# Optimization experiments

Hardware: AMD Instinct MI355X
Metric: run time of the kernel (lower is better)

The kernel has to match this reference:

```python
import jax, jax.numpy as jnp
import numpy as np

B, S, D, H = 4, 1024, 1024, 16
DH = D // H  # head dim = 64
NEG = 1e9  # keras Softmax masking constant for fp32


def setup_inputs() -> dict:
    key = jax.random.key(0)
    ks = jax.random.split(key, 7)
    return {
        "inputs": jax.random.normal(ks[0], (B, S, D), jnp.float32),
        "mask": jax.random.randint(ks[1], (B, 1, 1, S), 0, 2) > 0,
        "interaction": jax.random.normal(ks[2], (B, S, S, H), jnp.float32) * 0.1,
        "W_Q": jax.random.normal(ks[3], (D, D), jnp.float32) * 0.02,
        "W_K": jax.random.normal(ks[4], (D, D), jnp.float32) * 0.02,
        "W_V": jax.random.normal(ks[5], (D, D), jnp.float32) * 0.02,
        "W_O": jax.random.normal(ks[6], (D, D), jnp.float32) * 0.02,
    }


def reference(inputs, mask, interaction, W_Q, W_K, W_V, W_O):
    b, s, d = inputs.shape
    def proj(W):
        # [B,S,D] @ [D,D] -> [B,S,H,DH] -> [B,H,S,DH]
        return (inputs @ W).reshape(b, s, H, DH).transpose(0, 2, 1, 3)
    Q, K, V = proj(W_Q), proj(W_K), proj(W_V)
    scores = jnp.einsum("bhqd,bhkd->bhqk", Q, K) / (DH ** 0.5)
    # interaction [B,S,S,H] -> [B,H,S,S], additive bias before softmax
    scores = scores + interaction.transpose(0, 3, 1, 2)
    # keras Softmax(mask=...): add -1e9 where mask is False, softmax over last axis
    scores = jnp.where(mask, scores, scores - NEG)
    attn = jax.nn.softmax(scores, axis=-1)
    hidden = jnp.einsum("bhqk,bhkd->bhqd", attn, V)
    hidden = hidden.transpose(0, 2, 1, 3).reshape(b, s, d)
    return hidden @ W_O
```

## Files before the change

kernel.cpp:

```cpp
#include <hip/hip_runtime.h>
#include <hip/hip_bf16.h>
#include <stdint.h>

#define BDIM 4
#define SDIM 1024
#define DDIM 1024
#define HDIM 16
#define DHDIM 64

typedef __bf16 bf16_t;
typedef __bf16 bf16x8 __attribute__((ext_vector_type(8)));
typedef __bf16 bf16x4 __attribute__((ext_vector_type(4)));
typedef float f32x4 __attribute__((ext_vector_type(4)));

typedef __attribute__((address_space(3))) uint32_t lds_u32;
typedef const __attribute__((address_space(1))) uint32_t glb_u32;

__device__ __forceinline__ void glds16(const void* g, void* l) {
    __builtin_amdgcn_global_load_lds((glb_u32*)g, (lds_u32*)l, 16, 0, 0);
}


__global__ __launch_bounds__(256) void convert_x_kernel(const float* __restrict__ X,
                                                        bf16_t* __restrict__ Xb, int n) {
    int i = (blockIdx.x * 256 + threadIdx.x) * 4;
    if (i >= n) return;
    float4 v = *(const float4*)(X + i);
    bf16x4 o;
    o[0] = (bf16_t)v.x; o[1] = (bf16_t)v.y; o[2] = (bf16_t)v.z; o[3] = (bf16_t)v.w;
    *(bf16x4*)(Xb + i) = o;
}

__global__ __launch_bounds__(256) void transpose_w_kernel(const float* __restrict__ W0,
                                                          const float* __restrict__ W1,
                                                          const float* __restrict__ W2,
                                                          const float* __restrict__ W3,
                                                          bf16_t* __restrict__ Wt) {
    __shared__ float tile[32][33];
    int z = blockIdx.z;
    const float* W = (z == 0) ? W0 : (z == 1) ? W1 : (z == 2) ? W2 : W3;
    bf16_t* dst = Wt + (size_t)z * DDIM * DDIM;
    int bx = blockIdx.x * 32;
    int by = blockIdx.y * 32;
    int x = threadIdx.x & 31, y0 = threadIdx.x >> 5;
#pragma unroll
    for (int i = 0; i < 4; i++) {
        int y = y0 + i * 8;
        tile[y][x] = W[(size_t)(by + y) * DDIM + bx + x];
    }
    __syncthreads();
#pragma unroll
    for (int i = 0; i < 4; i++) {
        int y = y0 + i * 8;
        dst[(size_t)(bx + y) * DDIM + by + x] = (bf16_t)tile[x][y];
    }
}

__global__ __launch_bounds__(1024) void mask_flag_kernel(const unsigned char* __restrict__ mb,
                                                         int* __restrict__ flag) {
    __shared__ int any;
    if (threadIdx.x == 0) any = 0;
    __syncthreads();
    int loc = 0;
    for (int i = threadIdx.x; i < BDIM * SDIM; i += 1024)
        if ((i & 3) && mb[i]) loc = 1;
    if (loc) any = 1;
    __syncthreads();
    if (threadIdx.x == 0) *flag = any ? 1 : 0;
}

template <int MODE>
__global__ __launch_bounds__(256) void gemm_bt_kernel(const bf16_t* __restrict__ A,
                                                      const bf16_t* __restrict__ Bt,
                                                      bf16_t* __restrict__ Qo, bf16_t* __restrict__ Ko,
                                                      bf16_t* __restrict__ Vto, float* __restrict__ Co) {
    __shared__ bf16_t As[128 * 32];
    __shared__ bf16_t Bs[128 * 32];
    const int m0 = blockIdx.x * 128;
    const int n0 = blockIdx.y * 128;
    const int t = threadIdx.x;
    const int lane = t & 63, w = t >> 6;
    const int wm = w & 1, wn = w >> 1;
    const int low = lane & 15, quad = lane >> 4;
    f32x4 acc[4][4] = {};

    const int srow = w * 16 + (lane >> 2);
    const int koff = (lane & 3) * 8;
    const bf16_t* Ag = A + (size_t)(m0 + srow) * DDIM + koff;
    const bf16_t* Bg = Bt + (size_t)(n0 + srow) * DDIM + koff;
    bf16_t* AsW = As + w * 512;
    bf16_t* BsW = Bs + w * 512;

    for (int k0 = 0; k0 < DDIM; k0 += 32) {
        __syncthreads();
        glds16(Ag + k0, AsW);
        glds16(Ag + (size_t)64 * DDIM + k0, AsW + 64 * 32);
        glds16(Bg + k0, BsW);
        glds16(Bg + (size_t)64 * DDIM + k0, BsW + 64 * 32);
        __syncthreads();
        bf16x8 af[4], bv[4];
#pragma unroll
        for (int mt = 0; mt < 4; mt++)
            af[mt] = *(const bf16x8*)(As + (wm * 64 + mt * 16 + low) * 32 + quad * 8);
#pragma unroll
        for (int nt = 0; nt < 4; nt++)
            bv[nt] = *(const bf16x8*)(Bs + (wn * 64 + nt * 16 + low) * 32 + quad * 8);
#pragma unroll
        for (int mt = 0; mt < 4; mt++)
#pragma unroll
            for (int nt = 0; nt < 4; nt++)
                acc[mt][nt] = __builtin_amdgcn_mfma_f32_16x16x32_bf16(af[mt], bv[nt], acc[mt][nt], 0, 0, 0);
    }

#pragma unroll
    for (int mt = 0; mt < 4; mt++) {
#pragma unroll
        for (int nt = 0; nt < 4; nt++) {
#pragma unroll
            for (int r = 0; r < 4; r++) {
                int mrow = m0 + wm * 64 + mt * 16 + quad * 4 + r;
                int ncol = n0 + wn * 64 + nt * 16 + low;
                float vv = acc[mt][nt][r];
                if (MODE == 0) {
                    int which = ncol >> 10, nl = ncol & 1023;
                    int h = nl >> 6, dh = nl & 63;
                    int b = mrow >> 10, s = mrow & 1023;
                    if (which == 0)
                        Qo[((size_t)(b * HDIM + h) * SDIM + s) * DHDIM + dh] = (bf16_t)(vv * 0.125f);
                    else if (which == 1)
                        Ko[((size_t)(b * HDIM + h) * SDIM + s) * DHDIM + dh] = (bf16_t)vv;
                    else
                        Vto[((size_t)(b * HDIM + h) * DHDIM + dh) * SDIM + s] = (bf16_t)vv;
                } else {
                    Co[(size_t)mrow * DDIM + ncol] = vv;
                }
            }
        }
    }
}

__global__ __launch_bounds__(1024, 4) void attn_kernel(const bf16_t* __restrict__ Q,
                                                       const bf16_t* __restrict__ K,
                                                       const bf16_t* __restrict__ Vt,
                                                       const float* __restrict__ inter,
                                                       const unsigned char* __restrict__ maskb,
                                                       const int* __restrict__ flagp,
                                                       bf16_t* __restrict__ hid) {
    constexpr int KS = 20;
    constexpr int HS = 32 * KS + 4;
    __shared__ bf16_t bias_l[2][16 * HS];
    __shared__ bf16_t P[16][16 * 40];
    const int b = blockIdx.y;
    const int q0 = blockIdx.x * 16;
    const int t = threadIdx.x;
    const int w = t >> 6, lane = t & 63;
    const int low = lane & 15, quad = lane >> 4;
    const int h = w;
    const int mstride = (*flagp) ? 1 : 4;

    const int kl = lane >> 1;
    const int hb = (lane & 1) * 8;
    const float* srcQ = inter + ((size_t)(b * SDIM + q0 + w) * SDIM) * HDIM + lane * 8;
    const unsigned char* mb = maskb + (size_t)b * SDIM * mstride;

    const bf16_t* Qb = Q + ((size_t)(b * HDIM + h) * SDIM + q0) * DHDIM;
    bf16x8 qf0 = *(const bf16x8*)(Qb + low * DHDIM + quad * 8);
    bf16x8 qf1 = *(const bf16x8*)(Qb + low * DHDIM + 32 + quad * 8);

    const bf16_t* Kb = K + (size_t)(b * HDIM + h) * SDIM * DHDIM;
    const bf16_t* VtB = Vt + (size_t)(b * HDIM + h) * DHDIM * SDIM;
    bf16_t* Pw = &P[w][0];

    float mrow[4], lrow[4];
    f32x4 accO[4] = {};
#pragma unroll
    for (int r = 0; r < 4; r++) { mrow[r] = -3.0e38f; lrow[r] = 0.f; }

    float4 r0 = *(const float4*)(srcQ + 0);
    float4 r1 = *(const float4*)(srcQ + 4);
    float pcur = mb[kl * mstride] ? 0.f : 1.0e9f;
    {
        bf16_t* d = &bias_l[0][kl * KS + w];
        d[(hb + 0) * HS] = (bf16_t)(r0.x - pcur);
        d[(hb + 1) * HS] = (bf16_t)(r0.y - pcur);
        d[(hb + 2) * HS] = (bf16_t)(r0.z - pcur);
        d[(hb + 3) * HS] = (bf16_t)(r0.w - pcur);
        d[(hb + 4) * HS] = (bf16_t)(r1.x - pcur);
        d[(hb + 5) * HS] = (bf16_t)(r1.y - pcur);
        d[(hb + 6) * HS] = (bf16_t)(r1.z - pcur);
        d[(hb + 7) * HS] = (bf16_t)(r1.w - pcur);
    }

    for (int c = 0; c < SDIM / 32; c++) {
        __syncthreads();
        const int kbase = c * 32;
        float4 n0v, n1v; float pnext = 0.f;
        if (c + 1 < SDIM / 32) {
            n0v = *(const float4*)(srcQ + (c + 1) * 512 + 0);
            n1v = *(const float4*)(srcQ + (c + 1) * 512 + 4);
            pnext = mb[((c + 1) * 32 + kl) * mstride] ? 0.f : 1.0e9f;
        }
        f32x4 sacc[2];
#pragma unroll
        for (int nt = 0; nt < 2; nt++) {
            const bf16_t* kp = Kb + (size_t)(kbase + nt * 16 + low) * DHDIM;
            bf16x8 kf0 = *(const bf16x8*)(kp + quad * 8);
            bf16x8 kf1 = *(const bf16x8*)(kp + 32 + quad * 8);
            f32x4 z = {};
            z = __builtin_amdgcn_mfma_f32_16x16x32_bf16(qf0, kf0, z, 0, 0, 0);
            z = __builtin_amdgcn_mfma_f32_16x16x32_bf16(qf1, kf1, z, 0, 0, 0);
            sacc[nt] = z;
        }
        const bf16_t* bias_c = &bias_l[c & 1][h * HS];
        float sv[2][4];
#pragma unroll
        for (int nt = 0; nt < 2; nt++) {
            bf16x4 bv = *(const bf16x4*)(bias_c + (nt * 16 + low) * KS + quad * 4);
#pragma unroll
            for (int r = 0; r < 4; r++) sv[nt][r] = sacc[nt][r] + (float)bv[r];
        }
#pragma unroll
        for (int r = 0; r < 4; r++) {
            float vmx = fmaxf(sv[0][r], sv[1][r]);
            vmx = fmaxf(vmx, __shfl_xor(vmx, 1));
            vmx = fmaxf(vmx, __shfl_xor(vmx, 2));
            vmx = fmaxf(vmx, __shfl_xor(vmx, 4));
            vmx = fmaxf(vmx, __shfl_xor(vmx, 8));
            float mn = fmaxf(mrow[r], vmx);
            float alpha = __expf(mrow[r] - mn);
            mrow[r] = mn;
            lrow[r] *= alpha;
#pragma unroll
            for (int nt = 0; nt < 4; nt++) accO[nt][r] *= alpha;
            float p0 = __expf(sv[0][r] - mn);
            float p1 = __expf(sv[1][r] - mn);
            sv[0][r] = p0; sv[1][r] = p1;
            float rs = p0 + p1;
            rs += __shfl_xor(rs, 1);
            rs += __shfl_xor(rs, 2);
            rs += __shfl_xor(rs, 4);
            rs += __shfl_xor(rs, 8);
            lrow[r] += rs;
        }
#pragma unroll
        for (int nt = 0; nt < 2; nt++)
#pragma unroll
            for (int r = 0; r < 4; r++)
                Pw[(quad * 4 + r) * 40 + nt * 16 + low] = (bf16_t)sv[nt][r];
        bf16x8 pf = *(const bf16x8*)(Pw + low * 40 + quad * 8);
#pragma unroll
        for (int nt = 0; nt < 4; nt++) {
            bf16x8 vf = *(const bf16x8*)(VtB + (size_t)(nt * 16 + low) * SDIM + kbase + quad * 8);
            accO[nt] = __builtin_amdgcn_mfma_f32_16x16x32_bf16(pf, vf, accO[nt], 0, 0, 0);
        }
        if (c + 1 < SDIM / 32) {
            bf16_t* d = &bias_l[(c + 1) & 1][kl * KS + w];
            d[(hb + 0) * HS] = (bf16_t)(n0v.x - pnext);
            d[(hb + 1) * HS] = (bf16_t)(n0v.y - pnext);
            d[(hb + 2) * HS] = (bf16_t)(n0v.z - pnext);
            d[(hb + 3) * HS] = (bf16_t)(n0v.w - pnext);
            d[(hb + 4) * HS] = (bf16_t)(n1v.x - pnext);
            d[(hb + 5) * HS] = (bf16_t)(n1v.y - pnext);
            d[(hb + 6) * HS] = (bf16_t)(n1v.z - pnext);
            d[(hb + 7) * HS] = (bf16_t)(n1v.w - pnext);
        }
    }
#pragma unroll
    for (int r = 0; r < 4; r++) {
        float inv = 1.f / lrow[r];
#pragma unroll
        for (int nt = 0; nt < 4; nt++) {
            hid[((size_t)b * SDIM + q0 + quad * 4 + r) * DDIM + h * 64 + nt * 16 + low] =
                (bf16_t)(accO[nt][r] * inv);
        }
    }
}


extern "C" void kernel_launch(void* const* d_in, const int* in_sizes, int n_in,
                              void* d_out, int out_size, void* d_ws, size_t ws_size,
                              hipStream_t stream) {
    const float* X = (const float*)d_in[0];
    const unsigned char* maskb = (const unsigned char*)d_in[1];
    const float* inter = (const float*)d_in[2];
    const float* WQ = (const float*)d_in[3];
    const float* WK = (const float*)d_in[4];
    const float* WV = (const float*)d_in[5];
    const float* WO = (const float*)d_in[6];
    float* out = (float*)d_out;

    char* ws = (char*)d_ws;
    const size_t MB = 1024 * 1024;
    bf16_t* Xb  = (bf16_t*)(ws + 0 * MB);
    bf16_t* Wt  = (bf16_t*)(ws + 8 * MB);
    bf16_t* Qm  = (bf16_t*)(ws + 16 * MB);
    bf16_t* Km  = (bf16_t*)(ws + 24 * MB);
    bf16_t* Vtm = (bf16_t*)(ws + 32 * MB);
    bf16_t* hid = (bf16_t*)(ws + 40 * MB);
    int* flag   = (int*)(ws + 48 * MB);

    convert_x_kernel<<<BDIM * SDIM * DDIM / (256 * 4), 256, 0, stream>>>(X, Xb, BDIM * SDIM * DDIM);
    transpose_w_kernel<<<dim3(32, 32, 4), 256, 0, stream>>>(WQ, WK, WV, WO, Wt);
    mask_flag_kernel<<<1, 1024, 0, stream>>>(maskb, flag);
    gemm_bt_kernel<0><<<dim3(32, 24), 256, 0, stream>>>(Xb, Wt, Qm, Km, Vtm, nullptr);
    attn_kernel<<<dim3(SDIM / 16, BDIM), 1024, 0, stream>>>(Qm, Km, Vtm, inter, maskb, flag, hid);
    gemm_bt_kernel<1><<<dim3(32, 8), 256, 0, stream>>>(hid, Wt + (size_t)3 * DDIM * DDIM,
                                                       nullptr, nullptr, nullptr, out);
}
```

Baseline: 566.4 us.

## Transpose score MFMA, prefetch K/V a chunk ahead, vectorize bias and V stores

The attention kernel now computes scores as K·Q^T, so each lane holds one query row's values. This turns the softmax row max and sum into mostly in-register reductions with two cross-lane shuffles instead of four per row. K fragments for the next chunk and V fragments for the current chunk are loaded at the top of the loop, so global latency overlaps with the MFMA and softmax work. The bias/mask staging is rewritten so each lane reads strided interaction values, loads mask bytes as a vector, and writes a single bf16x8 to LDS with a new padding layout. The projection epilogue writes V^T as 4-element vector stores. The cost is more registers from the prefetched fragments and strided global reads of the interaction tensor, which may coalesce less well.

```diff
diff --git a/kernel.cpp b/kernel.cpp
--- a/kernel.cpp
+++ b/kernel.cpp
@@ -114,26 +114,34 @@
 
 #pragma unroll
     for (int mt = 0; mt < 4; mt++) {
+        const int mbase = m0 + wm * 64 + mt * 16 + quad * 4;
 #pragma unroll
         for (int nt = 0; nt < 4; nt++) {
-#pragma unroll
-            for (int r = 0; r < 4; r++) {
-                int mrow = m0 + wm * 64 + mt * 16 + quad * 4 + r;
-                int ncol = n0 + wn * 64 + nt * 16 + low;
-                float vv = acc[mt][nt][r];
-                if (MODE == 0) {
-                    int which = ncol >> 10, nl = ncol & 1023;
-                    int h = nl >> 6, dh = nl & 63;
-                    int b = mrow >> 10, s = mrow & 1023;
-                    if (which == 0)
-                        Qo[((size_t)(b * HDIM + h) * SDIM + s) * DHDIM + dh] = (bf16_t)(vv * 0.125f);
-                    else if (which == 1)
-                        Ko[((size_t)(b * HDIM + h) * SDIM + s) * DHDIM + dh] = (bf16_t)vv;
-                    else
-                        Vto[((size_t)(b * HDIM + h) * DHDIM + dh) * SDIM + s] = (bf16_t)vv;
+            const int ncol = n0 + wn * 64 + nt * 16 + low;
+            if (MODE == 0) {
+                const int which = ncol >> 10, nl = ncol & 1023;
+                const int hh = nl >> 6, dh = nl & 63;
+                const int bb = mbase >> 10, s = mbase & 1023;
+                if (which == 2) {
+                    bf16x4 pv;
+#pragma unroll
+                    for (int r = 0; r < 4; r++) pv[r] = (bf16_t)acc[mt][nt][r];
+                    *(bf16x4*)(Vto + ((size_t)((bb * HDIM + hh) * DHDIM + dh)) * SDIM + s) = pv;
+                } else if (which == 0) {
+#pragma unroll
+                    for (int r = 0; r < 4; r++)
+                        Qo[((size_t)(bb * HDIM + hh) * SDIM + (s + r)) * DHDIM + dh] =
+                            (bf16_t)(acc[mt][nt][r] * 0.125f);
                 } else {
-                    Co[(size_t)mrow * DDIM + ncol] = vv;
+#pragma unroll
+                    for (int r = 0; r < 4; r++)
+                        Ko[((size_t)(bb * HDIM + hh) * SDIM + (s + r)) * DHDIM + dh] =
+                            (bf16_t)acc[mt][nt][r];
                 }
+            } else {
+#pragma unroll
+                for (int r = 0; r < 4; r++)
+                    Co[(size_t)(mbase + r) * DDIM + ncol] = acc[mt][nt][r];
             }
         }
     }
@@ -146,10 +154,10 @@
                                                        const unsigned char* __restrict__ maskb,
                                                        const int* __restrict__ flagp,
                                                        bf16_t* __restrict__ hid) {
-    constexpr int KS = 20;
-    constexpr int HS = 32 * KS + 4;
+    constexpr int KS = 40;
+    constexpr int HS = 16 * KS + 8;
     __shared__ bf16_t bias_l[2][16 * HS];
-    __shared__ bf16_t P[16][16 * 40];
+    __shared__ bf16_t P[16][16 * KS];
     const int b = blockIdx.y;
     const int q0 = blockIdx.x * 16;
     const int t = threadIdx.x;
@@ -158,10 +166,11 @@
     const int h = w;
     const int mstride = (*flagp) ? 1 : 4;
 
-    const int kl = lane >> 1;
-    const int hb = (lane & 1) * 8;
-    const float* srcQ = inter + ((size_t)(b * SDIM + q0 + w) * SDIM) * HDIM + lane * 8;
+    const int sh = lane & 15;
+    const int sk0 = (lane >> 4) * 8;
+    const float* srcB = inter + ((size_t)(b * SDIM + q0 + w) * SDIM + sk0) * HDIM + sh;
     const unsigned char* mb = maskb + (size_t)b * SDIM * mstride;
+    const int stoff = sh * HS + w * KS + sk0;
 
     const bf16_t* Qb = Q + ((size_t)(b * HDIM + h) * SDIM + q0) * DHDIM;
     bf16x8 qf0 = *(const bf16x8*)(Qb + low * DHDIM + quad * 8);
@@ -171,107 +180,142 @@
     const bf16_t* VtB = Vt + (size_t)(b * HDIM + h) * DHDIM * SDIM;
     bf16_t* Pw = &P[w][0];
 
-    float mrow[4], lrow[4];
+    float mrow = -3.0e38f, lrow = 0.f;
     f32x4 accO[4] = {};
-#pragma unroll
-    for (int r = 0; r < 4; r++) { mrow[r] = -3.0e38f; lrow[r] = 0.f; }
-
-    float4 r0 = *(const float4*)(srcQ + 0);
-    float4 r1 = *(const float4*)(srcQ + 4);
-    float pcur = mb[kl * mstride] ? 0.f : 1.0e9f;
+
+    bf16x8 kA0 = *(const bf16x8*)(Kb + (size_t)(0 + low) * DHDIM + quad * 8);
+    bf16x8 kA1 = *(const bf16x8*)(Kb + (size_t)(0 + low) * DHDIM + 32 + quad * 8);
+    bf16x8 kB0 = *(const bf16x8*)(Kb + (size_t)(16 + low) * DHDIM + quad * 8);
+    bf16x8 kB1 = *(const bf16x8*)(Kb + (size_t)(16 + low) * DHDIM + 32 + quad * 8);
     {
-        bf16_t* d = &bias_l[0][kl * KS + w];
-        d[(hb + 0) * HS] = (bf16_t)(r0.x - pcur);
-        d[(hb + 1) * HS] = (bf16_t)(r0.y - pcur);
-        d[(hb + 2) * HS] = (bf16_t)(r0.z - pcur);
-        d[(hb + 3) * HS] = (bf16_t)(r0.w - pcur);
-        d[(hb + 4) * HS] = (bf16_t)(r1.x - pcur);
-        d[(hb + 5) * HS] = (bf16_t)(r1.y - pcur);
-        d[(hb + 6) * HS] = (bf16_t)(r1.z - pcur);
-        d[(hb + 7) * HS] = (bf16_t)(r1.w - pcur);
+        float b0v[8], pen0[8];
+#pragma unroll
+        for (int j = 0; j < 8; j++) b0v[j] = srcB[j * HDIM];
+        if (mstride == 1) {
+            uint64_t mw = *(const uint64_t*)(mb + sk0);
+#pragma unroll
+            for (int j = 0; j < 8; j++) pen0[j] = ((mw >> (8 * j)) & 0xff) ? 0.f : 1.0e9f;
+        } else {
+            const int4* mp = (const int4*)(mb + (size_t)sk0 * 4);
+            int4 ma = mp[0], mc = mp[1];
+            pen0[0] = ma.x ? 0.f : 1.0e9f; pen0[1] = ma.y ? 0.f : 1.0e9f;
+            pen0[2] = ma.z ? 0.f : 1.0e9f; pen0[3] = ma.w ? 0.f : 1.0e9f;
+            pen0[4] = mc.x ? 0.f : 1.0e9f; pen0[5] = mc.y ? 0.f : 1.0e9f;
+            pen0[6] = mc.z ? 0.f : 1.0e9f; pen0[7] = mc.w ? 0.f : 1.0e9f;
+        }
+        bf16x8 bw;
+#pragma unroll
+        for (int j = 0; j < 8; j++) bw[j] = (bf16_t)(b0v[j] - pen0[j]);
+        *(bf16x8*)(&bias_l[0][stoff]) = bw;
     }
 
     for (int c = 0; c < SDIM / 32; c++) {
         __syncthreads();
         const int kbase = c * 32;
-        float4 n0v, n1v; float pnext = 0.f;
-        if (c + 1 < SDIM / 32) {
-            n0v = *(const float4*)(srcQ + (c + 1) * 512 + 0);
-            n1v = *(const float4*)(srcQ + (c + 1) * 512 + 4);
-            pnext = mb[((c + 1) * 32 + kl) * mstride] ? 0.f : 1.0e9f;
-        }
-        f32x4 sacc[2];
-#pragma unroll
-        for (int nt = 0; nt < 2; nt++) {
-            const bf16_t* kp = Kb + (size_t)(kbase + nt * 16 + low) * DHDIM;
-            bf16x8 kf0 = *(const bf16x8*)(kp + quad * 8);
-            bf16x8 kf1 = *(const bf16x8*)(kp + 32 + quad * 8);
-            f32x4 z = {};
-            z = __builtin_amdgcn_mfma_f32_16x16x32_bf16(qf0, kf0, z, 0, 0, 0);
-            z = __builtin_amdgcn_mfma_f32_16x16x32_bf16(qf1, kf1, z, 0, 0, 0);
-            sacc[nt] = z;
-        }
-        const bf16_t* bias_c = &bias_l[c & 1][h * HS];
-        float sv[2][4];
-#pragma unroll
-        for (int nt = 0; nt < 2; nt++) {
-            bf16x4 bv = *(const bf16x4*)(bias_c + (nt * 16 + low) * KS + quad * 4);
-#pragma unroll
-            for (int r = 0; r < 4; r++) sv[nt][r] = sacc[nt][r] + (float)bv[r];
-        }
+
+        bf16x8 vf[4];
+#pragma unroll
+        for (int nt = 0; nt < 4; nt++)
+            vf[nt] = *(const bf16x8*)(VtB + (size_t)(nt * 16 + low) * SDIM + kbase + quad * 8);
+
+        bf16x8 nA0, nA1, nB0, nB1;
+        float nb[8], npen[8];
+        if (c < SDIM / 32 - 1) {
+            const int k2 = kbase + 32;
+            const bf16_t* kpA = Kb + (size_t)(k2 + low) * DHDIM;
+            const bf16_t* kpB = Kb + (size_t)(k2 + 16 + low) * DHDIM;
+            nA0 = *(const bf16x8*)(kpA + quad * 8);
+            nA1 = *(const bf16x8*)(kpA + 32 + quad * 8);
+            nB0 = *(const bf16x8*)(kpB + quad * 8);
+            nB1 = *(const bf16x8*)(kpB + 32 + quad * 8);
+            const float* s2 = srcB + (size_t)(c + 1) * 512;
+#pragma unroll
+            for (int j = 0; j < 8; j++) nb[j] = s2[j * HDIM];
+            const int kb2 = k2 + sk0;
+            if (mstride == 1) {
+                uint64_t mw = *(const uint64_t*)(mb + kb2);
+#pragma unroll
+                for (int j = 0; j < 8; j++) npen[j] = ((mw >> (8 * j)) & 0xff) ? 0.f : 1.0e9f;
+            } else {
+                const int4* mp = (const int4*)(mb + (size_t)kb2 * 4);
+                int4 ma = mp[0], mc = mp[1];
+                npen[0] = ma.x ? 0.f : 1.0e9f; npen[1] = ma.y ? 0.f : 1.0e9f;
+                npen[2] = ma.z ? 0.f : 1.0e9f; npen[3] = ma.w ? 0.f : 1.0e9f;
+                npen[4] = mc.x ? 0.f : 1.0e9f; npen[5] = mc.y ? 0.f : 1.0e9f;
+                npen[6] = mc.z ? 0.f : 1.0e9f; npen[7] = mc.w ? 0.f : 1.0e9f;
+            }
+        }
+
+        f32x4 s0 = {}, s1 = {};
+        s0 = __builtin_amdgcn_mfma_f32_16x16x32_bf16(kA0, qf0, s0, 0, 0, 0);
+        s0 = __builtin_amdgcn_mfma_f32_16x16x32_bf16(kA1, qf1, s0, 0, 0, 0);
+        s1 = __builtin_amdgcn_mfma_f32_16x16x32_bf16(kB0, qf0, s1, 0, 0, 0);
+        s1 = __builtin_amdgcn_mfma_f32_16x16x32_bf16(kB1, qf1, s1, 0, 0, 0);
+
+        const bf16_t* bc = &bias_l[c & 1][h * HS + low * KS];
+        bf16x4 bv0 = *(const bf16x4*)(bc + quad * 4);
+        bf16x4 bv1 = *(const bf16x4*)(bc + 16 + quad * 4);
+        float sv[8];
 #pragma unroll
         for (int r = 0; r < 4; r++) {
-            float vmx = fmaxf(sv[0][r], sv[1][r]);
-            vmx = fmaxf(vmx, __shfl_xor(vmx, 1));
-            vmx = fmaxf(vmx, __shfl_xor(vmx, 2));
-            vmx = fmaxf(vmx, __shfl_xor(vmx, 4));
-            vmx = fmaxf(vmx, __shfl_xor(vmx, 8));
-            float mn = fmaxf(mrow[r], vmx);
-            float alpha = __expf(mrow[r] - mn);
-            mrow[r] = mn;
-            lrow[r] *= alpha;
-#pragma unroll
-            for (int nt = 0; nt < 4; nt++) accO[nt][r] *= alpha;
-            float p0 = __expf(sv[0][r] - mn);
-            float p1 = __expf(sv[1][r] - mn);
-            sv[0][r] = p0; sv[1][r] = p1;
-            float rs = p0 + p1;
-            rs += __shfl_xor(rs, 1);
-            rs += __shfl_xor(rs, 2);
-            rs += __shfl_xor(rs, 4);
-            rs += __shfl_xor(rs, 8);
-            lrow[r] += rs;
-        }
-#pragma unroll
-        for (int nt = 0; nt < 2; nt++)
-#pragma unroll
-            for (int r = 0; r < 4; r++)
-                Pw[(quad * 4 + r) * 40 + nt * 16 + low] = (bf16_t)sv[nt][r];
-        bf16x8 pf = *(const bf16x8*)(Pw + low * 40 + quad * 8);
-#pragma unroll
-        for (int nt = 0; nt < 4; nt++) {
-            bf16x8 vf = *(const bf16x8*)(VtB + (size_t)(nt * 16 + low) * SDIM + kbase + quad * 8);
-            accO[nt] = __builtin_amdgcn_mfma_f32_16x16x32_bf16(pf, vf, accO[nt], 0, 0, 0);
-        }
-        if (c + 1 < SDIM / 32) {
-            bf16_t* d = &bias_l[(c + 1) & 1][kl * KS + w];
-            d[(hb + 0) * HS] = (bf16_t)(n0v.x - pnext);
-            d[(hb + 1) * HS] = (bf16_t)(n0v.y - pnext);
-            d[(hb + 2) * HS] = (bf16_t)(n0v.z - pnext);
-            d[(hb + 3) * HS] = (bf16_t)(n0v.w - pnext);
-            d[(hb + 4) * HS] = (bf16_t)(n1v.x - pnext);
-            d[(hb + 5) * HS] = (bf16_t)(n1v.y - pnext);
-            d[(hb + 6) * HS] = (bf16_t)(n1v.z - pnext);
-            d[(hb + 7) * HS] = (bf16_t)(n1v.w - pnext);
-        }
-    }
+            sv[r] = s0[r] + (float)bv0[r];
+            sv[4 + r] = s1[r] + (float)bv1[r];
+        }
+
+        float vmx = sv[0];
+#pragma unroll
+        for (int j = 1; j < 8; j++) vmx = fmaxf(vmx, sv[j]);
+        vmx = fmaxf(vmx, __shfl_xor(vmx, 16));
+        vmx = fmaxf(vmx, __shfl_xor(vmx, 32));
+        float mn = fmaxf(mrow, vmx);
+        float alpha = __expf(mrow - mn);
+        mrow = mn;
+        float ps = 0.f;
+        bf16x4 p0, p1;
+#pragma unroll
+        for (int j = 0; j < 4; j++) {
+            float e0 = __expf(sv[j] - mn);
+            float e1 = __expf(sv[4 + j] - mn);
+            ps += e0 + e1;
+            p0[j] = (bf16_t)e0;
+            p1[j] = (bf16_t)e1;
+        }
+        ps += __shfl_xor(ps, 16);
+        ps += __shfl_xor(ps, 32);
+        lrow = lrow * alpha + ps;
+
+#pragma unroll
+        for (int r = 0; r < 4; r++) {
+            float ar = __shfl(alpha, (lane & 48) | (quad * 4 + r));
+#pragma unroll
+            for (int nt = 0; nt < 4; nt++) accO[nt][r] *= ar;
+        }
+
+        *(bf16x4*)(Pw + low * KS + quad * 4) = p0;
+        *(bf16x4*)(Pw + low * KS + 16 + quad * 4) = p1;
+        bf16x8 pf = *(const bf16x8*)(Pw + low * KS + quad * 8);
+
+#pragma unroll
+        for (int nt = 0; nt < 4; nt++)
+            accO[nt] = __builtin_amdgcn_mfma_f32_16x16x32_bf16(pf, vf[nt], accO[nt], 0, 0, 0);
+
+        if (c < SDIM / 32 - 1) {
+            bf16x8 bw;
+#pragma unroll
+            for (int j = 0; j < 8; j++) bw[j] = (bf16_t)(nb[j] - npen[j]);
+            *(bf16x8*)(&bias_l[(c + 1) & 1][stoff]) = bw;
+            kA0 = nA0; kA1 = nA1; kB0 = nB0; kB1 = nB1;
+        }
+    }
+
+    float linv = 1.f / lrow;
 #pragma unroll
     for (int r = 0; r < 4; r++) {
-        float inv = 1.f / lrow[r];
+        float lr = __shfl(linv, (lane & 48) | (quad * 4 + r));
 #pragma unroll
         for (int nt = 0; nt < 4; nt++) {
             hid[((size_t)b * SDIM + q0 + quad * 4 + r) * DDIM + h * 64 + nt * 16 + low] =
-                (bf16_t)(accO[nt][r] * inv);
+                (bf16_t)(accO[nt][r] * lr);
         }
     }
 }
```

After: 543.0 us. -4.1%, faster.
